# Optimization experiments

Measured on AMD Instinct MI355X. Metric: run time of the kernel, lower is better.

Reference implementation:

```python
import jax, jax.numpy as jnp
import numpy as np

B, D, F = 2048, 512, 16384
K = 3
AUX_THR = 0.7
EPS = 1e-8


def setup_inputs() -> dict:
    key = jax.random.key(0)
    ks = jax.random.split(key, 14)
    sc_e = 1.0 / np.sqrt(D)
    sc_d = 1.0 / np.sqrt(F)
    return {
        "model_activations": jax.random.normal(ks[0], (B, D), jnp.float32),
        "We": jax.random.normal(ks[1], (F, D), jnp.float32) * sc_e,
        "be": jax.random.normal(ks[2], (F,), jnp.float32) * 0.01,
        "Wd": jax.random.normal(ks[3], (D, F), jnp.float32) * sc_d,
        "bd": jax.random.normal(ks[4], (D,), jnp.float32) * 0.01,
        "We1": jax.random.normal(ks[5], (F, D), jnp.float32) * sc_e,
        "be1": jax.random.normal(ks[6], (F,), jnp.float32) * 0.01,
        "Wd1": jax.random.normal(ks[7], (D, F), jnp.float32) * sc_d,
        "bd1": jax.random.normal(ks[8], (D,), jnp.float32) * 0.01,
        "We2": jax.random.normal(ks[9], (F, D), jnp.float32) * sc_e,
        "be2": jax.random.normal(ks[10], (F,), jnp.float32) * 0.01,
        "Wd2": jax.random.normal(ks[11], (D, F), jnp.float32) * sc_d,
        "bd2": jax.random.normal(ks[12], (D,), jnp.float32) * 0.01,
    }


def _forward(x, We, be, Wd, bd, We1, be1, Wd1, bd1, We2, be2, Wd2, bd2):
    # parent encoder + top-k scatter
    pre = x @ We.T + be                                   # [B, F]
    vals, idx = jax.lax.top_k(pre, K)                     # [B, K]
    sae = jnp.zeros_like(pre).at[jnp.arange(B)[:, None], idx].set(vals)

    # child routing
    pre1 = x @ We1.T + be1
    pre2 = x @ We2.T + be2
    sae_nz = sae != 0.0
    m1 = jnp.where(sae_nz, pre1, 0.0)
    m2 = jnp.where(sae_nz, pre2, 0.0)
    winners = m1 > m2
    fa1 = jnp.where(winners, m1, 0.0)
    fa2 = jnp.where(~winners, m2, 0.0)

    recon = (sae @ Wd.T + bd) + (fa1 @ Wd1.T + bd1) + (fa2 @ Wd2.T + bd2)

    # live-latent counts (as arrays, jit-friendly)
    n_parent = jnp.zeros((F,), jnp.float32).at[idx.reshape(-1)].set(1.0).sum().astype(jnp.int32)
    n_c1 = jnp.any(fa1 != 0, axis=0).sum().astype(jnp.int32)
    n_c2 = jnp.any(fa2 != 0, axis=0).sum().astype(jnp.int32)

    # auxiliary cosine loss, computed per-feature without materializing
    # the [B, D, F] scaled_parent / combined_weights tensors:
    #   scaled_parent[b,:,f] = a * Wd[:,f],  scaled_child[b,:,f] = c * Wc[:,f]
    # cos over D reduces to per-feature Gram terms.
    pp = jnp.sum(Wd * Wd, axis=0)      # [F] ||Wp_f||^2
    p1 = jnp.sum(Wd * Wd1, axis=0)     # [F] Wp_f . W1_f
    p2 = jnp.sum(Wd * Wd2, axis=0)
    s11 = jnp.sum(Wd1 * Wd1, axis=0)
    s22 = jnp.sum(Wd2 * Wd2, axis=0)

    a = sae                                              # [B, F]
    c = jnp.where(winners, fa1, fa2)                     # [B, F]
    pc = jnp.where(winners, p1[None, :], p2[None, :])    # [B, F]
    cc = jnp.where(winners, s11[None, :], s22[None, :])

    dot = a * (a * pp[None, :] + c * pc)                 # <scaled_parent, combined>
    nx = jnp.abs(a) * jnp.sqrt(pp)[None, :]              # ||scaled_parent||
    ny2 = a * a * pp[None, :] + 2.0 * a * c * pc + c * c * cc
    ny = jnp.sqrt(jnp.maximum(ny2, 0.0))                 # ||combined||
    cos = dot / (jnp.maximum(nx, EPS) * jnp.maximum(ny, EPS))

    active = (a > 0).astype(cos.dtype)
    sim_loss = jnp.maximum(0.0, AUX_THR - cos) * active
    aux = sim_loss.sum() / (active.sum() + 1e-08)

    return recon, (n_parent, n_c1, n_c2), aux


def reference(model_activations, We, be, Wd, bd, We1, be1, Wd1, bd1, We2, be2, Wd2, bd2):
    return _forward(model_activations, We, be, Wd, bd, We1, be1, Wd1, bd1, We2, be2, Wd2, bd2)
```

## Files before the change

kernel.cpp:

```cpp
#include <hip/hip_runtime.h>
#include <math.h>

#define B_DIM 2048
#define D_DIM 512
#define F_DIM 16384
#define K_TOP 3

typedef __attribute__((ext_vector_type(8))) short bf16x8;
typedef __attribute__((ext_vector_type(4))) float f32x4;

#define GL16(gsrc, ldst) \
  __builtin_amdgcn_global_load_lds( \
      (__attribute__((address_space(1))) const void*)(gsrc), \
      (__attribute__((address_space(3))) void*)(ldst), 16, 0, 0)

#define WAITVMCNT(n) asm volatile("s_waitcnt vmcnt(" #n ")" ::: "memory")
#define BARRIER() do { asm volatile("" ::: "memory"); \
    __builtin_amdgcn_s_barrier(); \
    asm volatile("" ::: "memory"); } while (0)

__device__ __forceinline__ bool better(float v, int c, float w, int j) {
    return (v > w) || (v == w && c < j);
}

__device__ __forceinline__ void ins3(float v, int c,
    float& v0, int& i0, float& v1, int& i1, float& v2, int& i2)
{
    if (!better(v, c, v2, i2)) return;
    if (better(v, c, v1, i1)) {
        v2 = v1; i2 = i1;
        if (better(v, c, v0, i0)) { v1 = v0; i1 = i0; v0 = v; i0 = c; }
        else { v1 = v; i1 = c; }
    } else { v2 = v; i2 = c; }
}

__device__ __forceinline__ uint okey(uint b16, int col) {
    uint m = 0x8000u + ((b16 >> 15) * 0x7FFFu);
    return ((b16 ^ m) << 14) | (uint)(16383 - col);
}

__device__ __forceinline__ void insK8(uint k, uint* V) {
#pragma unroll
    for (int j = 0; j < 8; ++j) {
        uint hi = V[j] > k ? V[j] : k;
        uint lo = V[j] > k ? k : V[j];
        V[j] = hi; k = lo;
    }
}

__device__ __forceinline__ void insK3(uint k, uint& V0, uint& V1, uint& V2) {
    uint h0 = V0 > k ? V0 : k, l0 = V0 > k ? k : V0; V0 = h0; k = l0;
    uint h1 = V1 > k ? V1 : k, l1 = V1 > k ? k : V1; V1 = h1; k = l1;
    V2 = V2 > k ? V2 : k;
}

__device__ __forceinline__ float bf2f(ushort u) {
    return __uint_as_float((uint)u << 16);
}

__global__ __launch_bounds__(256) void convert_kernel(
    const float* __restrict__ We, ushort* __restrict__ We_bf,
    const float* __restrict__ x, ushort* __restrict__ x_bf)
{
    const float* src; ushort* dst; int n8, i, stride;
    if (blockIdx.x < 2048) {
        src = We; dst = We_bf; n8 = F_DIM * D_DIM / 8;
        i = blockIdx.x * 256 + threadIdx.x; stride = 2048 * 256;
    } else {
        src = x; dst = x_bf; n8 = B_DIM * D_DIM / 8;
        i = (blockIdx.x - 2048) * 256 + threadIdx.x; stride = 256 * 256;
    }
    for (; i < n8; i += stride) {
        float4 a = ((const float4*)src)[i * 2];
        float4 b = ((const float4*)src)[i * 2 + 1];
        uint4 o;
        o.x = (__float_as_uint(a.y) & 0xFFFF0000u) | (__float_as_uint(a.x) >> 16);
        o.y = (__float_as_uint(a.w) & 0xFFFF0000u) | (__float_as_uint(a.z) >> 16);
        o.z = (__float_as_uint(b.y) & 0xFFFF0000u) | (__float_as_uint(b.x) >> 16);
        o.w = (__float_as_uint(b.w) & 0xFFFF0000u) | (__float_as_uint(b.z) >> 16);
        ((uint4*)dst)[i] = o;
    }
}

__global__ __launch_bounds__(256) void gemm_kernel(
    const ushort* __restrict__ xb, const ushort* __restrict__ web,
    const float* __restrict__ be, uint* __restrict__ packed)
{
    __shared__ __align__(16) ushort As[2][4096];
    __shared__ __align__(16) ushort Bs[2][4096];

    const int t = threadIdx.x;
    const int l = t & 63;
    const int w = t >> 6;
    const int wr = w >> 1, wc = w & 1;
    const int bm0 = blockIdx.y << 7;
    const int fn0 = blockIdx.x << 7;
    const int frow = l & 15;
    const int q = l >> 4;

    const int srow = t >> 2;
    const int sgr = (t & 3) ^ ((t >> 3) & 3);
    const int soff = sgr << 3;
    const ushort* gA0 = xb + (size_t)(bm0 + srow) * D_DIM + soff;
    const ushort* gA1 = xb + (size_t)(bm0 + 64 + srow) * D_DIM + soff;
    const ushort* gB0 = web + (size_t)(fn0 + srow) * D_DIM + soff;
    const ushort* gB1 = web + (size_t)(fn0 + 64 + srow) * D_DIM + soff;

#define STAGE(bufp, koff) do { \
    GL16(gA0 + (koff), (char*)As + (bufp) * 8192 + t * 16); \
    GL16(gA1 + (koff), (char*)As + (bufp) * 8192 + 4096 + t * 16); \
    GL16(gB0 + (koff), (char*)Bs + (bufp) * 8192 + t * 16); \
    GL16(gB1 + (koff), (char*)Bs + (bufp) * 8192 + 4096 + t * 16); \
} while (0)

    f32x4 acc[4][4];
#pragma unroll
    for (int m = 0; m < 4; ++m)
#pragma unroll
        for (int n = 0; n < 4; ++n) acc[m][n] = (f32x4)(0.f);

    const int qs = (q ^ ((frow >> 1) & 3)) << 3;
    const int aoff = (wr * 64 + frow) * 32 + qs;
    const int boff = (wc * 64 + frow) * 32 + qs;

    STAGE(0, 0);

#pragma unroll 1
    for (int t16 = 0; t16 < 16; ++t16) {
        const int cur = t16 & 1;
        if (t16 < 15) {
            STAGE(cur ^ 1, (t16 + 1) * 32);
            WAITVMCNT(4);
        } else {
            WAITVMCNT(0);
        }
        BARRIER();
        const ushort* Ab = &As[0][0] + cur * 4096 + aoff;
        const ushort* Bb = &Bs[0][0] + cur * 4096 + boff;
        bf16x8 af[4], bfr[4];
#pragma unroll
        for (int m = 0; m < 4; ++m) af[m] = *(const bf16x8*)(Ab + m * 512);
#pragma unroll
        for (int n = 0; n < 4; ++n) bfr[n] = *(const bf16x8*)(Bb + n * 512);
#pragma unroll
        for (int m = 0; m < 4; ++m)
#pragma unroll
            for (int n = 0; n < 4; ++n)
                acc[m][n] = __builtin_amdgcn_mfma_f32_16x16x32_bf16(
                    af[m], bfr[n], acc[m][n], 0, 0, 0);
        BARRIER();
    }
#undef STAGE

    float bias[4];
#pragma unroll
    for (int n = 0; n < 4; ++n) bias[n] = be[fn0 + wc * 64 + n * 16 + frow];

    const int colb = fn0 + wc * 64 + frow;
    const int rowbase = bm0 + wr * 64 + (q << 2);
    const int tile2 = (blockIdx.x << 1) + wc;
#pragma unroll
    for (int m = 0; m < 4; ++m) {
#pragma unroll
        for (int i = 0; i < 4; ++i) {
            uint V0 = 0, V1 = 0, V2 = 0;
#pragma unroll
            for (int n = 0; n < 4; ++n) {
                float v = acc[m][n][i] + bias[n];
                uint key = okey(__float_as_uint(v) >> 16, colb + n * 16);
                insK3(key, V0, V1, V2);
            }
#pragma unroll
            for (int mk = 1; mk <= 8; mk <<= 1) {
                uint o0 = (uint)__shfl_xor((int)V0, mk);
                uint o1 = (uint)__shfl_xor((int)V1, mk);
                uint o2 = (uint)__shfl_xor((int)V2, mk);
                insK3(o0, V0, V1, V2);
                insK3(o1, V0, V1, V2);
                insK3(o2, V0, V1, V2);
            }
            if (frow == 0) {
                uint* dp = packed + (size_t)(rowbase + m * 16 + i) * 768 + tile2 * 3;
                dp[0] = V0; dp[1] = V1; dp[2] = V2;
            }
        }
    }
}

__global__ __launch_bounds__(512) void trgram_kernel(
    const float* __restrict__ Wd, const float* __restrict__ Wd1,
    const float* __restrict__ Wd2, ushort* __restrict__ WdT,
    ushort* __restrict__ Wd1T, ushort* __restrict__ Wd2T,
    float* __restrict__ gram, int* __restrict__ flags3F)
{
    if (threadIdx.x < 48)
        ((uint4*)flags3F)[blockIdx.x * 48 + threadIdx.x] = make_uint4(0, 0, 0, 0);

    __shared__ float tA[64][65], tB[64][65], tC[64][65];
    __shared__ float gred[8][64][5];
    const int t = threadIdx.x;
    const int f0 = blockIdx.x << 6;
    const int wg = t >> 6;
    const int fl = t & 63;
    float pp = 0, p1 = 0, p2 = 0, s11 = 0, s22 = 0;

    for (int ch = 0; ch < 8; ++ch) {
        const int d0 = ch << 6;
        float a[8], b[8], c[8];
#pragma unroll
        for (int it = 0; it < 8; ++it) {
            int dl = (it << 3) + wg;
            size_t off = (size_t)(d0 + dl) * F_DIM + f0 + fl;
            a[it] = Wd[off]; b[it] = Wd1[off]; c[it] = Wd2[off];
        }
        if (ch) __syncthreads();
#pragma unroll
        for (int it = 0; it < 8; ++it) {
            pp  = fmaf(a[it], a[it], pp);
            p1  = fmaf(a[it], b[it], p1);
            p2  = fmaf(a[it], c[it], p2);
            s11 = fmaf(b[it], b[it], s11);
            s22 = fmaf(c[it], c[it], s22);
            int dl = (it << 3) + wg;
            tA[dl][fl] = a[it]; tB[dl][fl] = b[it]; tC[dl][fl] = c[it];
        }
        __syncthreads();
#pragma unroll
        for (int it = 0; it < 8; ++it) {
            int flw = (it << 3) + wg, dlw = fl;
            size_t doff = (size_t)(f0 + flw) * D_DIM + d0 + dlw;
            WdT[doff]  = (ushort)(__float_as_uint(tA[dlw][flw]) >> 16);
            Wd1T[doff] = (ushort)(__float_as_uint(tB[dlw][flw]) >> 16);
            Wd2T[doff] = (ushort)(__float_as_uint(tC[dlw][flw]) >> 16);
        }
    }
    gred[wg][fl][0] = pp;  gred[wg][fl][1] = p1; gred[wg][fl][2] = p2;
    gred[wg][fl][3] = s11; gred[wg][fl][4] = s22;
    __syncthreads();
    if (t < 64) {
        float g0 = 0, g1 = 0, g2 = 0, g3 = 0, g4 = 0;
#pragma unroll
        for (int g = 0; g < 8; ++g) {
            g0 += gred[g][t][0]; g1 += gred[g][t][1]; g2 += gred[g][t][2];
            g3 += gred[g][t][3]; g4 += gred[g][t][4];
        }
        gram[f0 + t] = g0;
        gram[F_DIM + f0 + t] = g1;
        gram[2 * F_DIM + f0 + t] = g2;
        gram[3 * F_DIM + f0 + t] = g3;
        gram[4 * F_DIM + f0 + t] = g4;
    }
}

__global__ __launch_bounds__(512) void mergerefine_kernel(
    const uint* __restrict__ packed,
    const float* __restrict__ x, const float* __restrict__ We,
    const float* __restrict__ be,
    float* __restrict__ vals, int* __restrict__ idxv)
{
    __shared__ int sc8[8];
    __shared__ float sv[8];
    __shared__ int si[8];
    const int row = blockIdx.x;
    const int t = threadIdx.x;

    if (t < 64) {
        const uint* p = packed + (size_t)row * 768;
        uint V[8] = {0, 0, 0, 0, 0, 0, 0, 0};
#pragma unroll
        for (int m = 0; m < 12; ++m) {
            uint k = p[t + (m << 6)];
            if (k > V[7]) insK8(k, V);
        }
#pragma unroll
        for (int mk = 1; mk < 64; mk <<= 1) {
            uint o[8];
#pragma unroll
            for (int j = 0; j < 8; ++j) o[j] = (uint)__shfl_xor((int)V[j], mk);
#pragma unroll
            for (int j = 0; j < 8; ++j)
                if (o[j] > V[7]) insK8(o[j], V);
        }
        if (t == 0) {
#pragma unroll
            for (int j = 0; j < 8; ++j)
                sc8[j] = 16383 - (int)(V[j] & 16383u);
        }
    }
    __syncthreads();

    const int wv = t >> 6, l = t & 63;
    const int f = sc8[wv];
    const float* xr = x + (size_t)row * D_DIM;
    const float* wp = We + (size_t)f * D_DIM;
    float s = 0.f;
#pragma unroll
    for (int m = 0; m < 8; ++m) { int e = l + (m << 6); s = fmaf(xr[e], wp[e], s); }
#pragma unroll
    for (int mk = 1; mk < 64; mk <<= 1) s += __shfl_xor(s, mk);
    if (l == 0) { sv[wv] = s + be[f]; si[wv] = f; }
    __syncthreads();
    if (t == 0) {
        float v0 = -INFINITY, v1 = -INFINITY, v2 = -INFINITY;
        int i0 = 0x7fffffff, i1 = 0x7fffffff, i2 = 0x7fffffff;
        for (int k = 0; k < 8; ++k) ins3(sv[k], si[k], v0, i0, v1, i1, v2, i2);
        vals[row * 3 + 0] = v0; idxv[row * 3 + 0] = i0;
        vals[row * 3 + 1] = v1; idxv[row * 3 + 1] = i1;
        vals[row * 3 + 2] = v2; idxv[row * 3 + 2] = i2;
    }
}

__global__ __launch_bounds__(512) void cra_kernel(
    const float* __restrict__ x,
    const float* __restrict__ We1, const float* __restrict__ be1,
    const float* __restrict__ We2, const float* __restrict__ be2,
    const float* __restrict__ vals, const int* __restrict__ idxv,
    const float* __restrict__ gram,
    const ushort* __restrict__ WdT, const float* __restrict__ bd,
    const ushort* __restrict__ Wd1T, const float* __restrict__ bd1,
    const ushort* __restrict__ Wd2T, const float* __restrict__ bd2,
    int* __restrict__ flagP, int* __restrict__ flag1, int* __restrict__ flag2,
    float* __restrict__ auxpart, float* __restrict__ cntpart,
    float* __restrict__ out)
{
    __shared__ float sval[3], sdot[3][2], scv[3], sterm[3], sact[3];
    __shared__ int sidx[3], swin[3];
    const int b = blockIdx.x;
    const int t = threadIdx.x;

    if (t < 3) { sidx[t] = idxv[b * 3 + t]; sval[t] = vals[b * 3 + t]; }
    __syncthreads();

    const int w = t >> 6, l = t & 63;
    if (w < 6) {
        const int p = w >> 1, mt = w & 1;
        const int f = sidx[p];
        const float* wp = (mt ? We2 : We1) + (size_t)f * D_DIM;
        const float* xr = x + (size_t)b * D_DIM;
        float s = 0.f;
#pragma unroll
        for (int m = 0; m < 8; ++m) { int e = l + (m << 6); s = fmaf(xr[e], wp[e], s); }
#pragma unroll
        for (int mk = 1; mk < 64; mk <<= 1) s += __shfl_xor(s, mk);
        if (l == 0) sdot[p][mt] = s + (mt ? be2 : be1)[f];
    }
    __syncthreads();

    if (t < 3) {
        const int p = t;
        const float a = sval[p];
        const int f = sidx[p];
        float m1 = (a != 0.f) ? sdot[p][0] : 0.f;
        float m2 = (a != 0.f) ? sdot[p][1] : 0.f;
        bool win = m1 > m2;
        float fa1 = win ? m1 : 0.f;
        float fa2 = win ? 0.f : m2;
        float cv = win ? fa1 : fa2;
        scv[p] = cv; swin[p] = win ? 1 : 0;
        flagP[f] = 1;
        if (fa1 != 0.f) flag1[f] = 1;
        if (fa2 != 0.f) flag2[f] = 1;
        const float pp = gram[f];
        const float pc = win ? gram[F_DIM + f] : gram[2 * F_DIM + f];
        const float cc = win ? gram[3 * F_DIM + f] : gram[4 * F_DIM + f];
        const float dot = a * (a * pp + cv * pc);
        const float nx = fabsf(a) * sqrtf(pp);
        const float ny2 = a * a * pp + 2.f * a * cv * pc + cv * cv * cc;
        const float ny = sqrtf(fmaxf(ny2, 0.f));
        const float cosv = dot / (fmaxf(nx, 1e-8f) * fmaxf(ny, 1e-8f));
        sterm[p] = (a > 0.f) ? fmaxf(0.f, 0.7f - cosv) : 0.f;
        sact[p] = (a > 0.f) ? 1.f : 0.f;
    }
    __syncthreads();
    if (t == 0) {
        auxpart[b] = sterm[0] + sterm[1] + sterm[2];
        cntpart[b] = sact[0] + sact[1] + sact[2];
    }

    const int d = t;
    float o = bd[d] + bd1[d] + bd2[d];
#pragma unroll
    for (int k = 0; k < 3; ++k) {
        const int f = sidx[k];
        const float a = sval[k];
        const float c = scv[k];
        const int win = swin[k];
        const size_t off = (size_t)f * D_DIM + d;
        o = fmaf(a, bf2f(WdT[off]), o);
        if (c != 0.f) {
            const ushort* wt = win ? Wd1T : Wd2T;
            o = fmaf(c, bf2f(wt[off]), o);
        }
    }
    out[(size_t)b * D_DIM + d] = o;
}

__global__ __launch_bounds__(256) void finalize_kernel(
    const int* __restrict__ flagP, const int* __restrict__ flag1,
    const int* __restrict__ flag2,
    const float* __restrict__ auxpart, const float* __restrict__ cntpart,
    float* __restrict__ out)
{
    const int t = threadIdx.x;
    int sp = 0, s1 = 0, s2 = 0;
    for (int f = t; f < F_DIM; f += 256) { sp += flagP[f]; s1 += flag1[f]; s2 += flag2[f]; }
    float asum = 0.f, acnt = 0.f;
    for (int i = t; i < B_DIM; i += 256) { asum += auxpart[i]; acnt += cntpart[i]; }
#pragma unroll
    for (int m = 1; m < 64; m <<= 1) {
        sp += __shfl_xor(sp, m); s1 += __shfl_xor(s1, m); s2 += __shfl_xor(s2, m);
        asum += __shfl_xor(asum, m); acnt += __shfl_xor(acnt, m);
    }
    __shared__ int red[3][4];
    __shared__ float fred[2][4];
    const int w = t >> 6;
    if ((t & 63) == 0) {
        red[0][w] = sp; red[1][w] = s1; red[2][w] = s2;
        fred[0][w] = asum; fred[1][w] = acnt;
    }
    __syncthreads();
    if (t == 0) {
        float np_ = (float)(red[0][0] + red[0][1] + red[0][2] + red[0][3]);
        float n1_ = (float)(red[1][0] + red[1][1] + red[1][2] + red[1][3]);
        float n2_ = (float)(red[2][0] + red[2][1] + red[2][2] + red[2][3]);
        float as = fred[0][0] + fred[0][1] + fred[0][2] + fred[0][3];
        float ac = fred[1][0] + fred[1][1] + fred[1][2] + fred[1][3];
        const size_t base = (size_t)B_DIM * D_DIM;
        out[base + 0] = np_;
        out[base + 1] = n1_;
        out[base + 2] = n2_;
        out[base + 3] = as / (ac + 1e-8f);
    }
}

extern "C" void kernel_launch(void* const* d_in, const int* in_sizes, int n_in,
                              void* d_out, int out_size, void* d_ws, size_t ws_size,
                              hipStream_t stream)
{
    (void)in_sizes; (void)n_in; (void)out_size; (void)ws_size;
    const float* x   = (const float*)d_in[0];
    const float* We  = (const float*)d_in[1];
    const float* be  = (const float*)d_in[2];
    const float* Wd  = (const float*)d_in[3];
    const float* bd  = (const float*)d_in[4];
    const float* We1 = (const float*)d_in[5];
    const float* be1 = (const float*)d_in[6];
    const float* Wd1 = (const float*)d_in[7];
    const float* bd1 = (const float*)d_in[8];
    const float* We2 = (const float*)d_in[9];
    const float* be2 = (const float*)d_in[10];
    const float* Wd2 = (const float*)d_in[11];
    const float* bd2 = (const float*)d_in[12];
    float* out = (float*)d_out;

    ushort* x_bf  = (ushort*)d_ws;
    ushort* We_bf = x_bf + (size_t)B_DIM * D_DIM;
    ushort* WdT   = We_bf + (size_t)F_DIM * D_DIM;
    ushort* Wd1T  = WdT + (size_t)F_DIM * D_DIM;
    ushort* Wd2T  = Wd1T + (size_t)F_DIM * D_DIM;
    uint*   packed = (uint*)(Wd2T + (size_t)F_DIM * D_DIM);
    float*  gram  = (float*)(packed + (size_t)B_DIM * 768);
    int*    flagP = (int*)(gram + 5 * F_DIM);
    int*    flag1 = flagP + F_DIM;
    int*    flag2 = flag1 + F_DIM;
    float*  vals  = (float*)(flag2 + F_DIM);
    int*    idxv  = (int*)(vals + B_DIM * 3);
    float*  auxpart = (float*)(idxv + B_DIM * 3);
    float*  cntpart = auxpart + B_DIM;

    convert_kernel<<<2304, 256, 0, stream>>>(We, We_bf, x, x_bf);

    dim3 g1(F_DIM / 128, B_DIM / 128);
    gemm_kernel<<<g1, 256, 0, stream>>>(x_bf, We_bf, be, packed);

    mergerefine_kernel<<<B_DIM, 512, 0, stream>>>(
        packed, x, We, be, vals, idxv);

    trgram_kernel<<<F_DIM / 64, 512, 0, stream>>>(
        Wd, Wd1, Wd2, WdT, Wd1T, Wd2T, gram, flagP);

    cra_kernel<<<B_DIM, 512, 0, stream>>>(
        x, We1, be1, We2, be2, vals, idxv, gram,
        WdT, bd, Wd1T, bd1, Wd2T, bd2,
        flagP, flag1, flag2, auxpart, cntpart, out);

    finalize_kernel<<<1, 256, 0, stream>>>(
        flagP, flag1, flag2, auxpart, cntpart, out);
}
```

Before: 143.2 us.

## Triple-buffer GEMM LDS pipeline and fuse merge-refine into routing kernel

The encoder GEMM moves from double to triple buffering, prefetching two K-slices ahead with adjusted vmcnt waits to hide more global-to-LDS latency. The separate merge/refine top-k kernel is folded into the child-routing/reconstruction kernel, so each row block does its own candidate merge, exact refinement and routing. This drops one launch and the vals/idx round trip through global memory. In exchange the GEMM uses more LDS per block, which may lower occupancy, and the fused kernel carries more serial work per block.

Measured after the change: 139.9 us. 1.02x faster.

```diff
diff --git a/kernel.cpp b/kernel.cpp
--- a/kernel.cpp
+++ b/kernel.cpp
@@ -86,8 +86,8 @@
     const ushort* __restrict__ xb, const ushort* __restrict__ web,
     const float* __restrict__ be, uint* __restrict__ packed)
 {
-    __shared__ __align__(16) ushort As[2][4096];
-    __shared__ __align__(16) ushort Bs[2][4096];
+    __shared__ __align__(16) ushort As[3][4096];
+    __shared__ __align__(16) ushort Bs[3][4096];
 
     const int t = threadIdx.x;
     const int l = t & 63;
@@ -124,12 +124,16 @@
     const int boff = (wc * 64 + frow) * 32 + qs;
 
     STAGE(0, 0);
-
+    STAGE(1, 32);
+
+    int cur = 0;
+    int nxt2 = 2;
 #pragma unroll 1
     for (int t16 = 0; t16 < 16; ++t16) {
-        const int cur = t16 & 1;
-        if (t16 < 15) {
-            STAGE(cur ^ 1, (t16 + 1) * 32);
+        if (t16 < 14) {
+            STAGE(nxt2, (t16 + 2) * 32);
+            WAITVMCNT(8);
+        } else if (t16 == 14) {
             WAITVMCNT(4);
         } else {
             WAITVMCNT(0);
@@ -149,6 +153,8 @@
                 acc[m][n] = __builtin_amdgcn_mfma_f32_16x16x32_bf16(
                     af[m], bfr[n], acc[m][n], 0, 0, 0);
         BARRIER();
+        cur = cur == 2 ? 0 : cur + 1;
+        nxt2 = nxt2 == 2 ? 0 : nxt2 + 1;
     }
 #undef STAGE
 
@@ -252,69 +258,12 @@
     }
 }
 
-__global__ __launch_bounds__(512) void mergerefine_kernel(
+__global__ __launch_bounds__(512) void mrcra_kernel(
     const uint* __restrict__ packed,
     const float* __restrict__ x, const float* __restrict__ We,
     const float* __restrict__ be,
-    float* __restrict__ vals, int* __restrict__ idxv)
-{
-    __shared__ int sc8[8];
-    __shared__ float sv[8];
-    __shared__ int si[8];
-    const int row = blockIdx.x;
-    const int t = threadIdx.x;
-
-    if (t < 64) {
-        const uint* p = packed + (size_t)row * 768;
-        uint V[8] = {0, 0, 0, 0, 0, 0, 0, 0};
-#pragma unroll
-        for (int m = 0; m < 12; ++m) {
-            uint k = p[t + (m << 6)];
-            if (k > V[7]) insK8(k, V);
-        }
-#pragma unroll
-        for (int mk = 1; mk < 64; mk <<= 1) {
-            uint o[8];
-#pragma unroll
-            for (int j = 0; j < 8; ++j) o[j] = (uint)__shfl_xor((int)V[j], mk);
-#pragma unroll
-            for (int j = 0; j < 8; ++j)
-                if (o[j] > V[7]) insK8(o[j], V);
-        }
-        if (t == 0) {
-#pragma unroll
-            for (int j = 0; j < 8; ++j)
-                sc8[j] = 16383 - (int)(V[j] & 16383u);
-        }
-    }
-    __syncthreads();
-
-    const int wv = t >> 6, l = t & 63;
-    const int f = sc8[wv];
-    const float* xr = x + (size_t)row * D_DIM;
-    const float* wp = We + (size_t)f * D_DIM;
-    float s = 0.f;
-#pragma unroll
-    for (int m = 0; m < 8; ++m) { int e = l + (m << 6); s = fmaf(xr[e], wp[e], s); }
-#pragma unroll
-    for (int mk = 1; mk < 64; mk <<= 1) s += __shfl_xor(s, mk);
-    if (l == 0) { sv[wv] = s + be[f]; si[wv] = f; }
-    __syncthreads();
-    if (t == 0) {
-        float v0 = -INFINITY, v1 = -INFINITY, v2 = -INFINITY;
-        int i0 = 0x7fffffff, i1 = 0x7fffffff, i2 = 0x7fffffff;
-        for (int k = 0; k < 8; ++k) ins3(sv[k], si[k], v0, i0, v1, i1, v2, i2);
-        vals[row * 3 + 0] = v0; idxv[row * 3 + 0] = i0;
-        vals[row * 3 + 1] = v1; idxv[row * 3 + 1] = i1;
-        vals[row * 3 + 2] = v2; idxv[row * 3 + 2] = i2;
-    }
-}
-
-__global__ __launch_bounds__(512) void cra_kernel(
-    const float* __restrict__ x,
     const float* __restrict__ We1, const float* __restrict__ be1,
     const float* __restrict__ We2, const float* __restrict__ be2,
-    const float* __restrict__ vals, const int* __restrict__ idxv,
     const float* __restrict__ gram,
     const ushort* __restrict__ WdT, const float* __restrict__ bd,
     const ushort* __restrict__ Wd1T, const float* __restrict__ bd1,
@@ -323,20 +272,67 @@
     float* __restrict__ auxpart, float* __restrict__ cntpart,
     float* __restrict__ out)
 {
+    __shared__ int sc8[8];
+    __shared__ float sv[8];
+    __shared__ int si[8];
     __shared__ float sval[3], sdot[3][2], scv[3], sterm[3], sact[3];
     __shared__ int sidx[3], swin[3];
-    const int b = blockIdx.x;
+    const int row = blockIdx.x;
     const int t = threadIdx.x;
-
-    if (t < 3) { sidx[t] = idxv[b * 3 + t]; sval[t] = vals[b * 3 + t]; }
-    __syncthreads();
-
-    const int w = t >> 6, l = t & 63;
-    if (w < 6) {
-        const int p = w >> 1, mt = w & 1;
+    const int wv = t >> 6, l = t & 63;
+
+    if (t < 64) {
+        const uint* p = packed + (size_t)row * 768;
+        uint V[8] = {0, 0, 0, 0, 0, 0, 0, 0};
+#pragma unroll
+        for (int m = 0; m < 12; ++m) {
+            uint k = p[t + (m << 6)];
+            if (k > V[7]) insK8(k, V);
+        }
+#pragma unroll
+        for (int mk = 1; mk < 64; mk <<= 1) {
+            uint o[8];
+#pragma unroll
+            for (int j = 0; j < 8; ++j) o[j] = (uint)__shfl_xor((int)V[j], mk);
+#pragma unroll
+            for (int j = 0; j < 8; ++j)
+                if (o[j] > V[7]) insK8(o[j], V);
+        }
+        if (t == 0) {
+#pragma unroll
+            for (int j = 0; j < 8; ++j)
+                sc8[j] = 16383 - (int)(V[j] & 16383u);
+        }
+    }
+    __syncthreads();
+
+    {
+        const int f = sc8[wv];
+        const float* xr = x + (size_t)row * D_DIM;
+        const float* wp = We + (size_t)f * D_DIM;
+        float s = 0.f;
+#pragma unroll
+        for (int m = 0; m < 8; ++m) { int e = l + (m << 6); s = fmaf(xr[e], wp[e], s); }
+#pragma unroll
+        for (int mk = 1; mk < 64; mk <<= 1) s += __shfl_xor(s, mk);
+        if (l == 0) { sv[wv] = s + be[f]; si[wv] = f; }
+    }
+    __syncthreads();
+    if (t == 0) {
+        float v0 = -INFINITY, v1 = -INFINITY, v2 = -INFINITY;
+        int i0 = 0x7fffffff, i1 = 0x7fffffff, i2 = 0x7fffffff;
+        for (int k = 0; k < 8; ++k) ins3(sv[k], si[k], v0, i0, v1, i1, v2, i2);
+        sval[0] = v0; sidx[0] = i0;
+        sval[1] = v1; sidx[1] = i1;
+        sval[2] = v2; sidx[2] = i2;
+    }
+    __syncthreads();
+
+    if (wv < 6) {
+        const int p = wv >> 1, mt = wv & 1;
         const int f = sidx[p];
         const float* wp = (mt ? We2 : We1) + (size_t)f * D_DIM;
-        const float* xr = x + (size_t)b * D_DIM;
+        const float* xr = x + (size_t)row * D_DIM;
         float s = 0.f;
 #pragma unroll
         for (int m = 0; m < 8; ++m) { int e = l + (m << 6); s = fmaf(xr[e], wp[e], s); }
@@ -373,8 +369,8 @@
     }
     __syncthreads();
     if (t == 0) {
-        auxpart[b] = sterm[0] + sterm[1] + sterm[2];
-        cntpart[b] = sact[0] + sact[1] + sact[2];
+        auxpart[row] = sterm[0] + sterm[1] + sterm[2];
+        cntpart[row] = sact[0] + sact[1] + sact[2];
     }
 
     const int d = t;
@@ -392,7 +388,7 @@
             o = fmaf(c, bf2f(wt[off]), o);
         }
     }
-    out[(size_t)b * D_DIM + d] = o;
+    out[(size_t)row * D_DIM + d] = o;
 }
 
 __global__ __launch_bounds__(256) void finalize_kernel(
@@ -463,9 +459,7 @@
     int*    flagP = (int*)(gram + 5 * F_DIM);
     int*    flag1 = flagP + F_DIM;
     int*    flag2 = flag1 + F_DIM;
-    float*  vals  = (float*)(flag2 + F_DIM);
-    int*    idxv  = (int*)(vals + B_DIM * 3);
-    float*  auxpart = (float*)(idxv + B_DIM * 3);
+    float*  auxpart = (float*)(flag2 + F_DIM);
     float*  cntpart = auxpart + B_DIM;
 
     convert_kernel<<<2304, 256, 0, stream>>>(We, We_bf, x, x_bf);
@@ -473,14 +467,11 @@
     dim3 g1(F_DIM / 128, B_DIM / 128);
     gemm_kernel<<<g1, 256, 0, stream>>>(x_bf, We_bf, be, packed);
 
-    mergerefine_kernel<<<B_DIM, 512, 0, stream>>>(
-        packed, x, We, be, vals, idxv);
-
     trgram_kernel<<<F_DIM / 64, 512, 0, stream>>>(
         Wd, Wd1, Wd2, WdT, Wd1T, Wd2T, gram, flagP);
 
-    cra_kernel<<<B_DIM, 512, 0, stream>>>(
-        x, We1, be1, We2, be2, vals, idxv, gram,
+    mrcra_kernel<<<B_DIM, 512, 0, stream>>>(
+        packed, x, We, be, We1, be1, We2, be2, gram,
         WdT, bd, Wd1T, bd1, Wd2T, bd2,
         flagP, flag1, flag2, auxpart, cntpart, out);
 
```
